# Optimization experiments

Hardware: AMD Instinct MI355X
Metric: run time of the kernel (lower is better)

## Reference

```python
import jax, jax.numpy as jnp
import numpy as np

N_NODES = 100000
N_EDGES = 1600000
IN_CH, HID_CH, OUT_CH = 512, 256, 64
K = 10
ALPHA = 0.1


def setup_inputs() -> dict:
    key = jax.random.key(0)
    k1, k2, k3, k4 = jax.random.split(key, 4)
    x = jax.random.normal(k1, (N_NODES, IN_CH), dtype=jnp.float32)
    edge_index = jax.random.randint(k2, (2, N_EDGES), 0, N_NODES, dtype=jnp.int64)
    w1 = jax.random.normal(k3, (IN_CH, HID_CH), dtype=jnp.float32) * 0.02
    b1 = jnp.zeros((HID_CH,), dtype=jnp.float32)
    w2 = jax.random.normal(k4, (HID_CH, OUT_CH), dtype=jnp.float32) * 0.02
    b2 = jnp.zeros((OUT_CH,), dtype=jnp.float32)
    return {"x": x, "edge_index": edge_index, "w1": w1, "b1": b1, "w2": w2, "b2": b2}


def reference(x, edge_index, w1, b1, w2, b2):
    n = x.shape[0]
    # MLP (dropout is identity in eval mode)
    h = jax.nn.relu(x @ w1 + b1)
    h = h @ w2 + b2  # [N, out]

    # GCN normalization with added self-loops (PyG gcn_norm)
    loops = jnp.arange(n, dtype=edge_index.dtype)
    src = jnp.concatenate([edge_index[0], loops])  # message sources (row)
    dst = jnp.concatenate([edge_index[1], loops])  # message targets (col)
    ones = jnp.ones(src.shape[0], dtype=h.dtype)
    deg = jax.ops.segment_sum(ones, dst, num_segments=n)
    dinv = jnp.where(deg > 0, jax.lax.rsqrt(deg), 0.0)
    norm = dinv[src] * dinv[dst]  # [E+N]

    h0 = h

    def step(hc, _):
        msg = jax.ops.segment_sum(norm[:, None] * hc[src], dst, num_segments=n)
        return (1.0 - ALPHA) * msg + ALPHA * h0, None

    h, _ = jax.lax.scan(step, h, None, length=K)
    return h
```

## Files before the change

### kernel.cpp

```cpp
#include <hip/hip_runtime.h>
#include <hip/hip_bf16.h>


typedef __attribute__((ext_vector_type(8))) short short8;
typedef __attribute__((ext_vector_type(4))) float floatx4;
typedef __attribute__((ext_vector_type(8))) _Float16 half8;

#define IN_CH 512
#define HID_CH 256
#define OUT_CH 64

static __device__ __forceinline__ unsigned short bf16_bits(float f) {
    __hip_bfloat16 b = __float2bfloat16(f);
    union { __hip_bfloat16 b; unsigned short u; } u2; u2.b = b; return u2.u;
}

typedef __attribute__((address_space(3))) unsigned int lds_u32;
typedef __attribute__((address_space(1))) const unsigned int glb_u32;

static __device__ __forceinline__ void gload16(const void* g, void* l) {
    __builtin_amdgcn_global_load_lds((glb_u32*)g, (lds_u32*)l, 16, 0, 0);
}

__global__ void k_probe(const int* __restrict__ e, long long ewords,
                        const unsigned short* __restrict__ xw,
                        int* __restrict__ meta) {
    if (blockIdx.x == 16) {
        int any = 0;
        long long half = ewords >> 1;
        long long step = half / 4096; if (step < 1) step = 1;
        for (long long i = threadIdx.x; i < 4096; i += blockDim.x) {
            long long idx = 2 * (i * step) + 1;
            if (idx < ewords) any |= e[idx];
        }
        if (any) atomicOr(&meta[0], 1);
    } else {
        const short8* x8 = (const short8*)xw;
        int bad = 0;
        for (int i = blockIdx.x * 256 + threadIdx.x; i < 8192; i += 4096) {
            short8 v = x8[i];
#pragma unroll
            for (int j = 0; j < 8; ++j) {
                unsigned short w = (unsigned short)v[j];
                if ((w & 0x7F80) == 0x7F80) bad = 1;
            }
        }
        if (bad) atomicOr(&meta[1], 1);
    }
}

__global__ void k_transpose(const void* __restrict__ w,
                            __hip_bfloat16* __restrict__ wt, int K, int N,
                            const int* __restrict__ meta) {
    int f32 = meta[1];
    int i = blockIdx.x * blockDim.x + threadIdx.x;
    if (i < K * N) {
        int k = i / N, n = i - k * N;
        __hip_bfloat16 v = f32 ? __float2bfloat16(((const float*)w)[i])
                               : ((const __hip_bfloat16*)w)[i];
        wt[n * K + k] = v;
    }
}

__global__ void k_count(const int* __restrict__ e, const int* __restrict__ meta,
                        int E, int* __restrict__ cnt, int* __restrict__ rank, int n) {
    int is32 = meta[0];
    int j = blockIdx.x * 256 + threadIdx.x;
    if (j < E) {
        long long idx = (long long)E + j;
        int d = is32 ? e[idx] : (int)((const long long*)e)[idx];
        if ((unsigned)d >= (unsigned)n) d = 0;
        rank[j] = atomicAdd(&cnt[d], 1);
    }
}

__global__ __launch_bounds__(1024) void k_scan1(const int* __restrict__ cnt,
                                                int* __restrict__ incl,
                                                int* __restrict__ bsum, int n) {
    __shared__ int s[1024];
    int i = blockIdx.x * 1024 + threadIdx.x;
    int v = (i < n) ? cnt[i] : 0;
    s[threadIdx.x] = v;
    __syncthreads();
    for (int off = 1; off < 1024; off <<= 1) {
        int t = (threadIdx.x >= off) ? s[threadIdx.x - off] : 0;
        __syncthreads();
        s[threadIdx.x] += t;
        __syncthreads();
    }
    incl[blockIdx.x * 1024 + threadIdx.x] = s[threadIdx.x];
    if (threadIdx.x == 1023) bsum[blockIdx.x] = s[1023];
}

__global__ void k_scan2(const int* __restrict__ bsum, int* __restrict__ boff, int nb) {
    if (blockIdx.x == 0 && threadIdx.x == 0) {
        int a = 0;
        for (int i = 0; i < nb; ++i) { boff[i] = a; a += bsum[i]; }
    }
}

__global__ void k_scan3(const int* __restrict__ incl, const int* __restrict__ cnt,
                        const int* __restrict__ boff, int* __restrict__ rowptr,
                        int n, int E) {
    int i = blockIdx.x * 256 + threadIdx.x;
    if (i < n) rowptr[i] = incl[i] - cnt[i] + boff[i >> 10];
    if (i == 0) rowptr[n] = E;
}

__global__ void k_dinv(const int* __restrict__ cnt, float* __restrict__ dinv, int n) {
    int i = blockIdx.x * 256 + threadIdx.x;
    if (i < n) dinv[i] = rsqrtf((float)cnt[i] + 1.0f);
}

__global__ void k_fill(const int* __restrict__ e, const int* __restrict__ meta, int E,
                       const int* __restrict__ rowptr, const int* __restrict__ rank,
                       int* __restrict__ col, int n) {
    int is32 = meta[0];
    int j = blockIdx.x * 256 + threadIdx.x;
    if (j < E) {
        int s, d;
        if (is32) { s = e[j]; d = e[(long long)E + j]; }
        else {
            const long long* e64 = (const long long*)e;
            s = (int)e64[j]; d = (int)e64[(long long)E + j];
        }
        if ((unsigned)s >= (unsigned)n) s = 0;
        if ((unsigned)d >= (unsigned)n) d = 0;
        col[rowptr[d] + rank[j]] = s;
    }
}

__global__ __launch_bounds__(1024, 4) void k_gemm1(
    const void* __restrict__ A, const __hip_bfloat16* __restrict__ Bt,
    const void* __restrict__ bias, __hip_bfloat16* __restrict__ C,
    int M, const int* __restrict__ meta)
{
    __shared__ __attribute__((aligned(16))) char lds[49152];
    const int f32 = meta[1];
    const int t = threadIdx.x;
    const int bm = blockIdx.x * 128;
    const int wave = t >> 6, lane = t & 63;
    const int wm = (wave & 3) * 32, wn = (wave >> 2) * 64;
    const int quad = lane >> 4, l16 = lane & 15;
    const int lrow = lane >> 3;
    const int lcol = ((lane & 7) ^ lrow) * 8;

    floatx4 acc[2][4];
#pragma unroll
    for (int i = 0; i < 2; ++i)
#pragma unroll
        for (int j = 0; j < 4; ++j) acc[i][j] = {0.f, 0.f, 0.f, 0.f};

    const __hip_bfloat16* Ab = (const __hip_bfloat16*)A;
    const float* Af = (const float*)A;

#define ABASE (lds)
#define BBASE (lds + 16384)

    int gr = bm + 8 * wave + lrow; if (gr >= M) gr = M - 1;

    for (int k0 = 0; k0 < IN_CH; k0 += 64) {
        __syncthreads();
#pragma unroll
        for (int i = 0; i < 2; ++i) {
            int s = wave * 2 + i;
            gload16(Bt + (size_t)(8 * s + lrow) * IN_CH + k0 + lcol,
                    BBASE + s * 1024);
        }
        if (f32) {
            const float* src = Af + (size_t)gr * IN_CH + k0 + lcol;
            float4 a = *(const float4*)src;
            float4 b = *(const float4*)(src + 4);
            union { short8 s8; unsigned short us[8]; } u;
            u.us[0] = bf16_bits(a.x); u.us[1] = bf16_bits(a.y);
            u.us[2] = bf16_bits(a.z); u.us[3] = bf16_bits(a.w);
            u.us[4] = bf16_bits(b.x); u.us[5] = bf16_bits(b.y);
            u.us[6] = bf16_bits(b.z); u.us[7] = bf16_bits(b.w);
            *(short8*)(ABASE + wave * 1024 + lane * 16) = u.s8;
        } else {
            gload16(Ab + (size_t)gr * IN_CH + k0 + lcol, ABASE + wave * 1024);
        }
        __syncthreads();
#pragma unroll
        for (int kk = 0; kk < 64; kk += 32) {
            const int cb = kk * 2 + quad * 16;
            short8 af[2], bf[4];
#pragma unroll
            for (int i = 0; i < 2; ++i) {
                int r = wm + i * 16 + l16;
                af[i] = *(const short8*)(ABASE + r * 128 + (cb ^ ((r & 7) << 4)));
            }
#pragma unroll
            for (int j = 0; j < 4; ++j) {
                int r = wn + j * 16 + l16;
                bf[j] = *(const short8*)(BBASE + r * 128 + (cb ^ ((r & 7) << 4)));
            }
#pragma unroll
            for (int i = 0; i < 2; ++i)
#pragma unroll
                for (int j = 0; j < 4; ++j)
                    acc[i][j] = __builtin_amdgcn_mfma_f32_16x16x32_bf16(af[i], bf[j], acc[i][j], 0, 0, 0);
        }
    }
#undef ABASE
#undef BBASE

#pragma unroll
    for (int i = 0; i < 2; ++i)
#pragma unroll
        for (int j = 0; j < 4; ++j) {
            int nn = wn + j * 16 + l16;
            float bv = f32 ? ((const float*)bias)[nn]
                           : __bfloat162float(((const __hip_bfloat16*)bias)[nn]);
#pragma unroll
            for (int r = 0; r < 4; ++r) {
                int m = bm + wm + i * 16 + quad * 4 + r;
                if (m < M)
                    C[(size_t)m * HID_CH + nn] = __float2bfloat16(fmaxf(acc[i][j][r] + bv, 0.f));
            }
        }
}

__global__ __launch_bounds__(256) void k_gemm2(
    const __hip_bfloat16* __restrict__ A, const __hip_bfloat16* __restrict__ Bt,
    const void* __restrict__ bias, const float* __restrict__ dinv,
    _Float16* __restrict__ h0h, _Float16* __restrict__ g0,
    int M, const int* __restrict__ meta)
{
    __shared__ __attribute__((aligned(16))) short As[64 * 72];
    __shared__ __attribute__((aligned(16))) short Bs[64 * 72];
    const int f32 = meta[1];
    const int t = threadIdx.x;
    const int bm = blockIdx.x * 64;
    const int wave = t >> 6, lane = t & 63;
    const int wm = (wave >> 1) * 32, wn = (wave & 1) * 32;
    const int quad = lane >> 4, l16 = lane & 15;

    floatx4 acc[2][2];
#pragma unroll
    for (int i = 0; i < 2; ++i)
#pragma unroll
        for (int j = 0; j < 2; ++j) acc[i][j] = {0.f, 0.f, 0.f, 0.f};

    for (int k0 = 0; k0 < HID_CH; k0 += 64) {
        __syncthreads();
        for (int ch = t; ch < 1024; ch += 256) {
            int row = (ch & 511) >> 3, off = (ch & 7) * 8;
            if (ch < 512) {
                uint4 av = {0u, 0u, 0u, 0u};
                int gr = bm + row;
                if (gr < M)
                    av = *(const uint4*)((const char*)A + ((size_t)gr * HID_CH + k0 + off) * 2);
                *(uint4*)((char*)As + row * 144 + off * 2) = av;
            } else {
                uint4 bv = *(const uint4*)((const char*)Bt + ((size_t)row * HID_CH + k0 + off) * 2);
                *(uint4*)((char*)Bs + row * 144 + off * 2) = bv;
            }
        }
        __syncthreads();
#pragma unroll
        for (int kk = 0; kk < 64; kk += 32) {
            short8 af[2], bf[2];
#pragma unroll
            for (int i = 0; i < 2; ++i)
                af[i] = *(const short8*)((const char*)As + (wm + i * 16 + l16) * 144 + (kk + quad * 8) * 2);
#pragma unroll
            for (int j = 0; j < 2; ++j)
                bf[j] = *(const short8*)((const char*)Bs + (wn + j * 16 + l16) * 144 + (kk + quad * 8) * 2);
#pragma unroll
            for (int i = 0; i < 2; ++i)
#pragma unroll
                for (int j = 0; j < 2; ++j)
                    acc[i][j] = __builtin_amdgcn_mfma_f32_16x16x32_bf16(af[i], bf[j], acc[i][j], 0, 0, 0);
        }
    }

#pragma unroll
    for (int i = 0; i < 2; ++i) {
#pragma unroll
        for (int j = 0; j < 2; ++j) {
            int nn = wn + j * 16 + l16;
            float bv = f32 ? ((const float*)bias)[nn]
                           : __bfloat162float(((const __hip_bfloat16*)bias)[nn]);
#pragma unroll
            for (int r = 0; r < 4; ++r) {
                int m = bm + wm + i * 16 + quad * 4 + r;
                if (m < M) {
                    float v = acc[i][j][r] + bv;
                    float dv = dinv[m];
                    h0h[(size_t)m * OUT_CH + nn] = (_Float16)v;
                    g0[(size_t)m * OUT_CH + nn] = (_Float16)(dv * v);
                }
            }
        }
    }
}

template<int FINAL>
__global__ __launch_bounds__(256) void k_prop(
    const _Float16* __restrict__ g, const _Float16* __restrict__ h0h,
    const int* __restrict__ rowptr, const int* __restrict__ col,
    const float* __restrict__ dinv,
    _Float16* __restrict__ gout, void* __restrict__ outfinal, int n,
    const int* __restrict__ meta)
{
    int gid = blockIdx.x * 32 + (threadIdx.x >> 3);
    if (gid >= n) return;
    int lane = threadIdx.x & 7;
    const half8* g8 = (const half8*)g;

    half8 sv = g8[(size_t)gid * 8 + lane];
    float acc[8];
#pragma unroll
    for (int i = 0; i < 8; ++i) acc[i] = (float)sv[i];

    int e0 = rowptr[gid], e1 = rowptr[gid + 1];
    int e = e0;
    for (; e + 8 <= e1; e += 8) {
        int c[8];
#pragma unroll
        for (int u = 0; u < 8; ++u) c[u] = col[e + u];
        half8 v[8];
#pragma unroll
        for (int u = 0; u < 8; ++u) v[u] = g8[(size_t)c[u] * 8 + lane];
#pragma unroll
        for (int u = 0; u < 8; ++u)
#pragma unroll
            for (int i = 0; i < 8; ++i) acc[i] += (float)v[u][i];
    }
    for (; e + 4 <= e1; e += 4) {
        int c0 = col[e], c1 = col[e + 1], c2 = col[e + 2], c3 = col[e + 3];
        half8 v0 = g8[(size_t)c0 * 8 + lane];
        half8 v1 = g8[(size_t)c1 * 8 + lane];
        half8 v2 = g8[(size_t)c2 * 8 + lane];
        half8 v3 = g8[(size_t)c3 * 8 + lane];
#pragma unroll
        for (int i = 0; i < 8; ++i)
            acc[i] += ((float)v0[i] + (float)v1[i]) + ((float)v2[i] + (float)v3[i]);
    }
    for (; e < e1; ++e) {
        half8 v = g8[(size_t)col[e] * 8 + lane];
#pragma unroll
        for (int i = 0; i < 8; ++i) acc[i] += (float)v[i];
    }

    float dv = dinv[gid];
    half8 z = ((const half8*)h0h)[(size_t)gid * 8 + lane];

    if (FINAL) {
        float o[8];
#pragma unroll
        for (int i = 0; i < 8; ++i) o[i] = 0.9f * dv * acc[i] + 0.1f * (float)z[i];
        if (meta[1]) {
            float* of = (float*)outfinal + (size_t)gid * OUT_CH + lane * 8;
            float4 a = {o[0], o[1], o[2], o[3]}, b = {o[4], o[5], o[6], o[7]};
            *(float4*)of = a; *(float4*)(of + 4) = b;
        } else {
            struct alignas(16) BF8 { unsigned short v[8]; } ob;
#pragma unroll
            for (int i = 0; i < 8; ++i) ob.v[i] = bf16_bits(o[i]);
            *(BF8*)((unsigned short*)outfinal + (size_t)gid * OUT_CH + lane * 8) = ob;
        }
    } else {
        float w2v = 0.9f * dv * dv, w1v = 0.1f * dv;
        half8 o;
#pragma unroll
        for (int i = 0; i < 8; ++i) o[i] = (_Float16)(w2v * acc[i] + w1v * (float)z[i]);
        ((half8*)gout)[(size_t)gid * 8 + lane] = o;
    }
}

extern "C" void kernel_launch(void* const* d_in, const int* in_sizes, int n_in,
                              void* d_out, int out_size, void* d_ws, size_t ws_size,
                              hipStream_t stream) {
    const void* x    = d_in[0];
    const int* edges = (const int*)d_in[1];
    const void* w1   = d_in[2];
    const void* b1   = d_in[3];
    const void* w2   = d_in[4];
    const void* b2   = d_in[5];

    const int N = in_sizes[0] / IN_CH;
    const int E = in_sizes[1] / 2;
    const int NB = (N + 1023) / 1024;

    size_t off = 0;
    auto carve = [&](size_t bytes) -> void* {
        void* r = (char*)d_ws + off;
        off += (bytes + 255) & ~(size_t)255;
        return r;
    };
    __hip_bfloat16* h1  = (__hip_bfloat16*)carve((size_t)N * HID_CH * 2);
    _Float16* h0h       = (_Float16*)carve((size_t)N * OUT_CH * 2);
    _Float16* gA        = (_Float16*)carve((size_t)N * OUT_CH * 2);
    _Float16* gB        = (_Float16*)carve((size_t)N * OUT_CH * 2);
    __hip_bfloat16* w1t = (__hip_bfloat16*)carve((size_t)IN_CH * HID_CH * 2);
    __hip_bfloat16* w2t = (__hip_bfloat16*)carve((size_t)HID_CH * OUT_CH * 2);
    int* cnt            = (int*)carve((size_t)N * 4);
    int* incl           = (int*)carve((size_t)NB * 1024 * 4);
    int* bsum           = (int*)carve(1024 * 4);
    int* boff           = (int*)carve(1024 * 4);
    int* rowptr         = (int*)carve((size_t)(N + 1) * 4);
    float* dinv         = (float*)carve((size_t)N * 4);
    int* col            = (int*)carve((size_t)E * 4);
    int* meta           = (int*)carve(256);
    if (off > ws_size) return;

    int* rank = (int*)h1;

    hipMemsetAsync(cnt, 0, (size_t)N * 4, stream);
    hipMemsetAsync(meta, 0, 8, stream);

    k_probe<<<17, 256, 0, stream>>>(edges, (long long)2 * E,
                                    (const unsigned short*)x, meta);

    k_transpose<<<(IN_CH * HID_CH + 255) / 256, 256, 0, stream>>>(w1, w1t, IN_CH, HID_CH, meta);
    k_transpose<<<(HID_CH * OUT_CH + 255) / 256, 256, 0, stream>>>(w2, w2t, HID_CH, OUT_CH, meta);

    const int EB = (E + 255) / 256;
    k_count<<<EB, 256, 0, stream>>>(edges, meta, E, cnt, rank, N);
    k_scan1<<<NB, 1024, 0, stream>>>(cnt, incl, bsum, N);
    k_scan2<<<1, 64, 0, stream>>>(bsum, boff, NB);
    k_scan3<<<(N + 255) / 256, 256, 0, stream>>>(incl, cnt, boff, rowptr, N, E);
    k_dinv<<<(N + 255) / 256, 256, 0, stream>>>(cnt, dinv, N);
    k_fill<<<EB, 256, 0, stream>>>(edges, meta, E, rowptr, rank, col, N);

    const int MB1 = (N + 127) / 128;
    k_gemm1<<<MB1, 1024, 0, stream>>>(x, w1t, b1, h1, N, meta);
    const int MB = (N + 63) / 64;
    k_gemm2<<<MB, 256, 0, stream>>>(h1, w2t, b2, dinv, h0h, gA, N, meta);

    const int PB = (N + 31) / 32;
    const _Float16* cur = gA;
    _Float16* nxt = gB;
    for (int it = 0; it < 10; ++it) {
        if (it < 9) {
            k_prop<0><<<PB, 256, 0, stream>>>(cur, h0h, rowptr, col, dinv, nxt, nullptr, N, meta);
            const _Float16* tmp = cur; cur = nxt; nxt = (_Float16*)tmp;
        } else {
            k_prop<1><<<PB, 256, 0, stream>>>(cur, h0h, rowptr, col, dinv, nullptr, d_out, N, meta);
        }
    }
}
```

Before: 815.1 us.

## Fuse both MLP GEMMs into one kernel and vectorize prop column loads

The two MLP GEMMs become one kernel. The ReLU'd hidden tile is written to LDS in bf16 with a swizzle, and the second GEMM reads it from there, so the N×256 intermediate no longer makes a round trip through global memory. The rank buffer gets its own workspace allocation because h1 no longer exists. In the propagation kernel, column indices are now loaded as int4 after a short loop that aligns to a multiple of four. LDS grows to 64KB per block, which may lower occupancy, and w2t is read straight from global memory by every block.

```diff
diff --git a/kernel.cpp b/kernel.cpp
--- a/kernel.cpp
+++ b/kernel.cpp
@@ -130,12 +130,14 @@
     }
 }
 
-__global__ __launch_bounds__(1024, 4) void k_gemm1(
+__global__ __launch_bounds__(1024, 4) void k_mlp(
     const void* __restrict__ A, const __hip_bfloat16* __restrict__ Bt,
-    const void* __restrict__ bias, __hip_bfloat16* __restrict__ C,
+    const void* __restrict__ bias1, const __hip_bfloat16* __restrict__ w2t,
+    const void* __restrict__ bias2, const float* __restrict__ dinv,
+    _Float16* __restrict__ h0h, _Float16* __restrict__ g0,
     int M, const int* __restrict__ meta)
 {
-    __shared__ __attribute__((aligned(16))) char lds[49152];
+    __shared__ __attribute__((aligned(16))) char lds[65536];
     const int f32 = meta[1];
     const int t = threadIdx.x;
     const int bm = blockIdx.x * 128;
@@ -205,92 +207,57 @@
 #undef ABASE
 #undef BBASE
 
+    __syncthreads();
 #pragma unroll
     for (int i = 0; i < 2; ++i)
 #pragma unroll
         for (int j = 0; j < 4; ++j) {
             int nn = wn + j * 16 + l16;
-            float bv = f32 ? ((const float*)bias)[nn]
-                           : __bfloat162float(((const __hip_bfloat16*)bias)[nn]);
+            float bv = f32 ? ((const float*)bias1)[nn]
+                           : __bfloat162float(((const __hip_bfloat16*)bias1)[nn]);
+            int cb = nn * 2;
 #pragma unroll
             for (int r = 0; r < 4; ++r) {
-                int m = bm + wm + i * 16 + quad * 4 + r;
-                if (m < M)
-                    C[(size_t)m * HID_CH + nn] = __float2bfloat16(fmaxf(acc[i][j][r] + bv, 0.f));
+                int row = wm + i * 16 + quad * 4 + r;
+                float v = fmaxf(acc[i][j][r] + bv, 0.f);
+                *(unsigned short*)(lds + row * 512 + (cb ^ ((row & 7) << 4))) = bf16_bits(v);
             }
         }
-}
-
-__global__ __launch_bounds__(256) void k_gemm2(
-    const __hip_bfloat16* __restrict__ A, const __hip_bfloat16* __restrict__ Bt,
-    const void* __restrict__ bias, const float* __restrict__ dinv,
-    _Float16* __restrict__ h0h, _Float16* __restrict__ g0,
-    int M, const int* __restrict__ meta)
-{
-    __shared__ __attribute__((aligned(16))) short As[64 * 72];
-    __shared__ __attribute__((aligned(16))) short Bs[64 * 72];
-    const int f32 = meta[1];
-    const int t = threadIdx.x;
-    const int bm = blockIdx.x * 64;
-    const int wave = t >> 6, lane = t & 63;
-    const int wm = (wave >> 1) * 32, wn = (wave & 1) * 32;
-    const int quad = lane >> 4, l16 = lane & 15;
-
-    floatx4 acc[2][2];
-#pragma unroll
-    for (int i = 0; i < 2; ++i)
-#pragma unroll
-        for (int j = 0; j < 2; ++j) acc[i][j] = {0.f, 0.f, 0.f, 0.f};
-
-    for (int k0 = 0; k0 < HID_CH; k0 += 64) {
-        __syncthreads();
-        for (int ch = t; ch < 1024; ch += 256) {
-            int row = (ch & 511) >> 3, off = (ch & 7) * 8;
-            if (ch < 512) {
-                uint4 av = {0u, 0u, 0u, 0u};
-                int gr = bm + row;
-                if (gr < M)
-                    av = *(const uint4*)((const char*)A + ((size_t)gr * HID_CH + k0 + off) * 2);
-                *(uint4*)((char*)As + row * 144 + off * 2) = av;
-            } else {
-                uint4 bv = *(const uint4*)((const char*)Bt + ((size_t)row * HID_CH + k0 + off) * 2);
-                *(uint4*)((char*)Bs + row * 144 + off * 2) = bv;
-            }
-        }
-        __syncthreads();
-#pragma unroll
-        for (int kk = 0; kk < 64; kk += 32) {
-            short8 af[2], bf[2];
-#pragma unroll
-            for (int i = 0; i < 2; ++i)
-                af[i] = *(const short8*)((const char*)As + (wm + i * 16 + l16) * 144 + (kk + quad * 8) * 2);
-#pragma unroll
-            for (int j = 0; j < 2; ++j)
-                bf[j] = *(const short8*)((const char*)Bs + (wn + j * 16 + l16) * 144 + (kk + quad * 8) * 2);
-#pragma unroll
-            for (int i = 0; i < 2; ++i)
-#pragma unroll
-                for (int j = 0; j < 2; ++j)
-                    acc[i][j] = __builtin_amdgcn_mfma_f32_16x16x32_bf16(af[i], bf[j], acc[i][j], 0, 0, 0);
-        }
-    }
-
-#pragma unroll
-    for (int i = 0; i < 2; ++i) {
+    __syncthreads();
+
+    const int wm2 = (wave & 7) * 16, wn2 = (wave >> 3) * 32;
+    floatx4 acc2[2];
+    acc2[0] = {0.f, 0.f, 0.f, 0.f};
+    acc2[1] = {0.f, 0.f, 0.f, 0.f};
+    const int ar = wm2 + l16;
+#pragma unroll
+    for (int kk = 0; kk < HID_CH; kk += 32) {
+        const int cbk = (kk + quad * 8) * 2;
+        short8 af = *(const short8*)(lds + ar * 512 + (cbk ^ ((ar & 7) << 4)));
+        short8 bf2[2];
 #pragma unroll
         for (int j = 0; j < 2; ++j) {
-            int nn = wn + j * 16 + l16;
-            float bv = f32 ? ((const float*)bias)[nn]
-                           : __bfloat162float(((const __hip_bfloat16*)bias)[nn]);
-#pragma unroll
-            for (int r = 0; r < 4; ++r) {
-                int m = bm + wm + i * 16 + quad * 4 + r;
-                if (m < M) {
-                    float v = acc[i][j][r] + bv;
-                    float dv = dinv[m];
-                    h0h[(size_t)m * OUT_CH + nn] = (_Float16)v;
-                    g0[(size_t)m * OUT_CH + nn] = (_Float16)(dv * v);
-                }
+            int nr = wn2 + j * 16 + l16;
+            bf2[j] = *(const short8*)((const char*)w2t + ((size_t)nr * HID_CH + kk + quad * 8) * 2);
+        }
+#pragma unroll
+        for (int j = 0; j < 2; ++j)
+            acc2[j] = __builtin_amdgcn_mfma_f32_16x16x32_bf16(af, bf2[j], acc2[j], 0, 0, 0);
+    }
+
+#pragma unroll
+    for (int j = 0; j < 2; ++j) {
+        int nn = wn2 + j * 16 + l16;
+        float bv = f32 ? ((const float*)bias2)[nn]
+                       : __bfloat162float(((const __hip_bfloat16*)bias2)[nn]);
+#pragma unroll
+        for (int r = 0; r < 4; ++r) {
+            int m = bm + wm2 + quad * 4 + r;
+            if (m < M) {
+                float v = acc2[j][r] + bv;
+                float dv = dinv[m];
+                h0h[(size_t)m * OUT_CH + nn] = (_Float16)v;
+                g0[(size_t)m * OUT_CH + nn] = (_Float16)(dv * v);
             }
         }
     }
@@ -316,24 +283,33 @@
 
     int e0 = rowptr[gid], e1 = rowptr[gid + 1];
     int e = e0;
+    for (; e < e1 && (e & 3); ++e) {
+        half8 v = g8[(size_t)col[e] * 8 + lane];
+#pragma unroll
+        for (int i = 0; i < 8; ++i) acc[i] += (float)v[i];
+    }
     for (; e + 8 <= e1; e += 8) {
-        int c[8];
-#pragma unroll
-        for (int u = 0; u < 8; ++u) c[u] = col[e + u];
-        half8 v[8];
-#pragma unroll
-        for (int u = 0; u < 8; ++u) v[u] = g8[(size_t)c[u] * 8 + lane];
-#pragma unroll
-        for (int u = 0; u < 8; ++u)
-#pragma unroll
-            for (int i = 0; i < 8; ++i) acc[i] += (float)v[u][i];
+        int4 ca = *(const int4*)(col + e);
+        int4 cb = *(const int4*)(col + e + 4);
+        half8 v0 = g8[(size_t)ca.x * 8 + lane];
+        half8 v1 = g8[(size_t)ca.y * 8 + lane];
+        half8 v2 = g8[(size_t)ca.z * 8 + lane];
+        half8 v3 = g8[(size_t)ca.w * 8 + lane];
+        half8 v4 = g8[(size_t)cb.x * 8 + lane];
+        half8 v5 = g8[(size_t)cb.y * 8 + lane];
+        half8 v6 = g8[(size_t)cb.z * 8 + lane];
+        half8 v7 = g8[(size_t)cb.w * 8 + lane];
+#pragma unroll
+        for (int i = 0; i < 8; ++i)
+            acc[i] += (((float)v0[i] + (float)v1[i]) + ((float)v2[i] + (float)v3[i]))
+                    + (((float)v4[i] + (float)v5[i]) + ((float)v6[i] + (float)v7[i]));
     }
     for (; e + 4 <= e1; e += 4) {
-        int c0 = col[e], c1 = col[e + 1], c2 = col[e + 2], c3 = col[e + 3];
-        half8 v0 = g8[(size_t)c0 * 8 + lane];
-        half8 v1 = g8[(size_t)c1 * 8 + lane];
-        half8 v2 = g8[(size_t)c2 * 8 + lane];
-        half8 v3 = g8[(size_t)c3 * 8 + lane];
+        int4 ca = *(const int4*)(col + e);
+        half8 v0 = g8[(size_t)ca.x * 8 + lane];
+        half8 v1 = g8[(size_t)ca.y * 8 + lane];
+        half8 v2 = g8[(size_t)ca.z * 8 + lane];
+        half8 v3 = g8[(size_t)ca.w * 8 + lane];
 #pragma unroll
         for (int i = 0; i < 8; ++i)
             acc[i] += ((float)v0[i] + (float)v1[i]) + ((float)v2[i] + (float)v3[i]);
@@ -390,7 +366,6 @@
         off += (bytes + 255) & ~(size_t)255;
         return r;
     };
-    __hip_bfloat16* h1  = (__hip_bfloat16*)carve((size_t)N * HID_CH * 2);
     _Float16* h0h       = (_Float16*)carve((size_t)N * OUT_CH * 2);
     _Float16* gA        = (_Float16*)carve((size_t)N * OUT_CH * 2);
     _Float16* gB        = (_Float16*)carve((size_t)N * OUT_CH * 2);
@@ -403,10 +378,9 @@
     int* rowptr         = (int*)carve((size_t)(N + 1) * 4);
     float* dinv         = (float*)carve((size_t)N * 4);
     int* col            = (int*)carve((size_t)E * 4);
+    int* rank           = (int*)carve((size_t)E * 4);
     int* meta           = (int*)carve(256);
     if (off > ws_size) return;
-
-    int* rank = (int*)h1;
 
     hipMemsetAsync(cnt, 0, (size_t)N * 4, stream);
     hipMemsetAsync(meta, 0, 8, stream);
@@ -426,9 +400,7 @@
     k_fill<<<EB, 256, 0, stream>>>(edges, meta, E, rowptr, rank, col, N);
 
     const int MB1 = (N + 127) / 128;
-    k_gemm1<<<MB1, 1024, 0, stream>>>(x, w1t, b1, h1, N, meta);
-    const int MB = (N + 63) / 64;
-    k_gemm2<<<MB, 256, 0, stream>>>(h1, w2t, b2, dinv, h0h, gA, N, meta);
+    k_mlp<<<MB1, 1024, 0, stream>>>(x, w1t, b1, w2t, b2, dinv, h0h, gA, N, meta);
 
     const int PB = (N + 31) / 32;
     const _Float16* cur = gA;
```

After: 838.8 us. 2.9% more time.
